# Kernel optimization log

Hardware: AMD Instinct MI355X
Metric: run time of the kernel (lower is better)

The kernel has to match this reference:

```python
import jax, jax.numpy as jnp
import numpy as np

N = 100000
E = 1600000

def _graphconv(x, src, dst, W, b):
    # DGL GraphConv, norm='both', in_feats > out_feats path: transform then aggregate.
    ones = jnp.ones((E,), dtype=x.dtype)
    out_deg = jax.ops.segment_sum(ones, src, num_segments=N)
    in_deg = jax.ops.segment_sum(ones, dst, num_segments=N)
    out_norm = jax.lax.rsqrt(jnp.clip(out_deg, 1.0))  # D_out^{-1/2}
    in_norm = jax.lax.rsqrt(jnp.clip(in_deg, 1.0))    # D_in^{-1/2}
    h = (x * out_norm[:, None]) @ W                    # [N, out_feats]
    msg = h[src]                                       # gather over edges [E, out_feats]
    agg = jax.ops.segment_sum(msg, dst, num_segments=N)
    return agg * in_norm[:, None] + b


def setup_inputs() -> dict:
    key = jax.random.key(0)
    k1, k2, k3, k4, k5 = jax.random.split(key, 5)
    features = jax.random.normal(k1, (N, 256), dtype=jnp.float32)
    src = jax.random.randint(k2, (E,), 0, N, dtype=jnp.int32)
    dst = jax.random.randint(k3, (E,), 0, N, dtype=jnp.int32)
    # Xavier-uniform like DGL's GraphConv reset_parameters
    lim1 = float(np.sqrt(6.0 / (256 + 64)))
    lim2 = float(np.sqrt(6.0 / (64 + 40)))
    W1 = jax.random.uniform(k4, (256, 64), jnp.float32, -lim1, lim1)
    W2 = jax.random.uniform(k5, (64, 40), jnp.float32, -lim2, lim2)
    b1 = jnp.zeros((64,), jnp.float32)
    b2 = jnp.zeros((40,), jnp.float32)
    return {"features": features, "src": src, "dst": dst,
            "W1": W1, "b1": b1, "W2": W2, "b2": b2}


def reference(features, src, dst, W1, b1, W2, b2):
    x = _graphconv(features, src, dst, W1, b1)
    x = _graphconv(x, src, dst, W2, b2)
    return x
```

## Files before the change

### kernel.cpp

```cpp
#include <hip/hip_runtime.h>

#define N_NODES 100000
#define N_EDGES 1600000
#define NBUCK 391
#define HBLK 128


__global__ __launch_bounds__(256) void coarse_hist_kernel(
    const int* __restrict__ src, const int* __restrict__ dst,
    int* __restrict__ gHD, int* __restrict__ gHS) {
    __shared__ int hd[NBUCK], hs[NBUCK];
    for (int i = threadIdx.x; i < NBUCK; i += 256) { hd[i] = 0; hs[i] = 0; }
    __syncthreads();
    for (int e = blockIdx.x * 256 + threadIdx.x; e < N_EDGES; e += HBLK * 256) {
        atomicAdd(&hd[dst[e] >> 8], 1);
        atomicAdd(&hs[src[e] >> 8], 1);
    }
    __syncthreads();
    for (int i = threadIdx.x; i < NBUCK; i += 256) {
        if (hd[i]) atomicAdd(&gHD[i], hd[i]);
        if (hs[i]) atomicAdd(&gHS[i], hs[i]);
    }
}


__global__ void coarse_scan_kernel(const int* __restrict__ gHD, const int* __restrict__ gHS,
                                   int* __restrict__ dBase, int* __restrict__ sBase) {
    __shared__ int sd[512], se[512];
    int t = threadIdx.x;
    int vd = (t < NBUCK) ? gHD[t] : 0;
    int vs = (t < NBUCK) ? gHS[t] : 0;
    sd[t] = vd; se[t] = vs;
    __syncthreads();
    for (int s = 1; s < 512; s <<= 1) {
        int ud = (t >= s) ? sd[t - s] : 0;
        int us = (t >= s) ? se[t - s] : 0;
        __syncthreads();
        sd[t] += ud; se[t] += us;
        __syncthreads();
    }
    if (t < NBUCK) { dBase[t] = sd[t] - vd; sBase[t] = se[t] - vs; }
    if (t == 0) { dBase[NBUCK] = N_EDGES; sBase[NBUCK] = N_EDGES; }
}


__global__ __launch_bounds__(256) void scatter_dst_kernel(
    const int* __restrict__ src, const int* __restrict__ dst,
    const int* __restrict__ dBase, int* __restrict__ dRes,
    int* __restrict__ bsrc, unsigned char* __restrict__ bdlo) {
    __shared__ int h[NBUCK];
    __shared__ int cur[NBUCK];
    for (int i = threadIdx.x; i < NBUCK; i += 256) h[i] = 0;
    __syncthreads();
    for (int e = blockIdx.x * 256 + threadIdx.x; e < N_EDGES; e += HBLK * 256)
        atomicAdd(&h[dst[e] >> 8], 1);
    __syncthreads();
    for (int i = threadIdx.x; i < NBUCK; i += 256) {
        int c = h[i];
        cur[i] = dBase[i] + (c ? atomicAdd(&dRes[i], c) : 0);
    }
    __syncthreads();
    for (int e = blockIdx.x * 256 + threadIdx.x; e < N_EDGES; e += HBLK * 256) {
        int d = dst[e];
        int p = atomicAdd(&cur[d >> 8], 1);
        bsrc[p] = src[e];
        bdlo[p] = (unsigned char)(d & 255);
    }
}


__global__ __launch_bounds__(256) void scatter_src_kernel(
    const int* __restrict__ src,
    const int* __restrict__ sBase, int* __restrict__ sRes,
    unsigned char* __restrict__ bslo) {
    __shared__ int h[NBUCK];
    __shared__ int cur[NBUCK];
    for (int i = threadIdx.x; i < NBUCK; i += 256) h[i] = 0;
    __syncthreads();
    for (int e = blockIdx.x * 256 + threadIdx.x; e < N_EDGES; e += HBLK * 256)
        atomicAdd(&h[src[e] >> 8], 1);
    __syncthreads();
    for (int i = threadIdx.x; i < NBUCK; i += 256) {
        int c = h[i];
        cur[i] = sBase[i] + (c ? atomicAdd(&sRes[i], c) : 0);
    }
    __syncthreads();
    for (int e = blockIdx.x * 256 + threadIdx.x; e < N_EDGES; e += HBLK * 256) {
        int s = src[e];
        int p = atomicAdd(&cur[s >> 8], 1);
        bslo[p] = (unsigned char)(s & 255);
    }
}


__global__ __launch_bounds__(256) void fine_dst_kernel(
    const int* __restrict__ dBase, const unsigned char* __restrict__ bdlo,
    const int* __restrict__ bsrc, int* __restrict__ rs, float* __restrict__ inorm,
    int* __restrict__ ssrc) {
    __shared__ int hist[256], scn[256], cur[256];
    int t = threadIdx.x, b = blockIdx.x;
    int lo = dBase[b], hi = dBase[b + 1];
    hist[t] = 0;
    __syncthreads();
    for (int p = lo + t; p < hi; p += 256) atomicAdd(&hist[bdlo[p]], 1);
    __syncthreads();
    int v = hist[t];
    scn[t] = v;
    __syncthreads();
    for (int s = 1; s < 256; s <<= 1) {
        int u = (t >= s) ? scn[t - s] : 0;
        __syncthreads();
        scn[t] += u;
        __syncthreads();
    }
    int excl = scn[t] - v;
    cur[t] = lo + excl;
    int node = b * 256 + t;
    if (node < N_NODES) {
        rs[node] = lo + excl;
        inorm[node] = 1.0f / sqrtf((float)max(v, 1));
    }
    if (b == 0 && t == 0) rs[N_NODES] = N_EDGES;
    __syncthreads();
    for (int p = lo + t; p < hi; p += 256) {
        int slot = atomicAdd(&cur[bdlo[p]], 1);
        ssrc[slot] = bsrc[p];
    }
}


__global__ __launch_bounds__(256) void fine_src_kernel(
    const int* __restrict__ sBase, const unsigned char* __restrict__ bslo,
    float* __restrict__ onorm) {
    __shared__ int hist[256];
    int t = threadIdx.x, b = blockIdx.x;
    int lo = sBase[b], hi = sBase[b + 1];
    hist[t] = 0;
    __syncthreads();
    for (int p = lo + t; p < hi; p += 256) atomicAdd(&hist[bslo[p]], 1);
    __syncthreads();
    int node = b * 256 + t;
    if (node < N_NODES) onorm[node] = 1.0f / sqrtf((float)max(hist[t], 1));
}


__global__ __launch_bounds__(256) void gemm1_kernel(
    const float* __restrict__ x, const float* __restrict__ W,
    const float* __restrict__ onorm, float* __restrict__ h, int n) {
    __shared__ float As[16][64];
    __shared__ float Ws[16][64];
    const int tid = threadIdx.x;
    const int tx = tid & 15;
    const int ty = tid >> 4;
    const int rowBase = blockIdx.x * 64;

    const int lr = tid >> 2;
    const int lk = (tid & 3) * 4;
    const int lrow = rowBase + lr;
    const bool lvalid = (lrow < n);
    const float lscale = lvalid ? onorm[lrow] : 0.0f;
    const int wk = tid >> 4;
    const int wc = (tid & 15) * 4;

    float acc[4][4] = {};

    for (int k0 = 0; k0 < 256; k0 += 16) {
        float4 v = make_float4(0.f, 0.f, 0.f, 0.f);
        if (lvalid) v = *(const float4*)(x + (size_t)lrow * 256 + k0 + lk);
        As[lk + 0][lr] = v.x * lscale;
        As[lk + 1][lr] = v.y * lscale;
        As[lk + 2][lr] = v.z * lscale;
        As[lk + 3][lr] = v.w * lscale;
        *(float4*)&Ws[wk][wc] = *(const float4*)(W + (size_t)(k0 + wk) * 64 + wc);
        __syncthreads();
#pragma unroll
        for (int k = 0; k < 16; ++k) {
            float4 a = *(const float4*)&As[k][ty * 4];
            float4 b = *(const float4*)&Ws[k][tx * 4];
            float av[4] = {a.x, a.y, a.z, a.w};
            float bv[4] = {b.x, b.y, b.z, b.w};
#pragma unroll
            for (int i = 0; i < 4; ++i)
#pragma unroll
                for (int j = 0; j < 4; ++j) acc[i][j] += av[i] * bv[j];
        }
        __syncthreads();
    }
#pragma unroll
    for (int i = 0; i < 4; ++i) {
        int row = rowBase + ty * 4 + i;
        if (row < n) {
            *(float4*)(h + (size_t)row * 64 + tx * 4) =
                make_float4(acc[i][0], acc[i][1], acc[i][2], acc[i][3]);
        }
    }
}


__global__ __launch_bounds__(256) void agg64_kernel(
    const int* __restrict__ rs, const int* __restrict__ ss,
    const float* __restrict__ h, float* __restrict__ agg, int n) {
    int node = (blockIdx.x * blockDim.x + threadIdx.x) >> 6;
    if (node >= n) return;
    int lane = threadIdx.x & 63;
    int q = lane >> 4;
    int f = lane & 15;
    int beg = rs[node], end = rs[node + 1];
    float4 a0 = {0.f, 0.f, 0.f, 0.f}, a1 = {0.f, 0.f, 0.f, 0.f};
    int j = beg;
    for (; j + 8 <= end; j += 8) {
        int s0 = ss[j + q];
        int s1 = ss[j + 4 + q];
        float4 v0 = *((const float4*)(h + (size_t)s0 * 64) + f);
        float4 v1 = *((const float4*)(h + (size_t)s1 * 64) + f);
        a0.x += v0.x; a0.y += v0.y; a0.z += v0.z; a0.w += v0.w;
        a1.x += v1.x; a1.y += v1.y; a1.z += v1.z; a1.w += v1.w;
    }
    for (; j + 4 <= end; j += 4) {
        int s0 = ss[j + q];
        float4 v0 = *((const float4*)(h + (size_t)s0 * 64) + f);
        a0.x += v0.x; a0.y += v0.y; a0.z += v0.z; a0.w += v0.w;
    }
    if (j + q < end) {
        int s0 = ss[j + q];
        float4 v0 = *((const float4*)(h + (size_t)s0 * 64) + f);
        a0.x += v0.x; a0.y += v0.y; a0.z += v0.z; a0.w += v0.w;
    }
    a0.x += a1.x; a0.y += a1.y; a0.z += a1.z; a0.w += a1.w;
    a0.x += __shfl_xor(a0.x, 16); a0.y += __shfl_xor(a0.y, 16);
    a0.z += __shfl_xor(a0.z, 16); a0.w += __shfl_xor(a0.w, 16);
    a0.x += __shfl_xor(a0.x, 32); a0.y += __shfl_xor(a0.y, 32);
    a0.z += __shfl_xor(a0.z, 32); a0.w += __shfl_xor(a0.w, 32);
    if (q == 0) ((float4*)(agg + (size_t)node * 64))[f] = a0;
}


__global__ __launch_bounds__(256) void gemm2_kernel(
    const float* __restrict__ agg, const float* __restrict__ W2,
    const float* __restrict__ b1, const float* __restrict__ inorm,
    const float* __restrict__ onorm, float* __restrict__ h2, int n) {
    __shared__ float Ws[64 * 40];
    int tid = threadIdx.x;
    for (int i = tid; i < 64 * 40; i += 256) Ws[i] = W2[i];
    __syncthreads();
    int lane = tid & 63;
    int wave = tid >> 6;
    int step = gridDim.x * 4;
    for (int row = blockIdx.x * 4 + wave; row < n; row += step) {
        float so  = onorm[row];
        float s12 = inorm[row] * so;
        const float* ar = agg + (size_t)row * 64;
        if (lane < 40) {
            float acc = 0.f;
#pragma unroll
            for (int k = 0; k < 64; ++k) {
                float xv = ar[k] * s12 + b1[k] * so;
                acc += xv * Ws[k * 40 + lane];
            }
            h2[(size_t)row * 40 + lane] = acc;
        }
    }
}


__global__ __launch_bounds__(256) void agg40_kernel(
    const int* __restrict__ rs, const int* __restrict__ ss,
    const float* __restrict__ h2, const float* __restrict__ inorm,
    const float* __restrict__ b2, float* __restrict__ out, int n) {
    int node = (blockIdx.x * blockDim.x + threadIdx.x) >> 6;
    if (node >= n) return;
    int lane = threadIdx.x & 63;
    int q = lane >> 4;
    int f = lane & 15;
    bool act = (f < 10);
    int beg = rs[node], end = rs[node + 1];
    float4 a0 = {0.f, 0.f, 0.f, 0.f}, a1 = {0.f, 0.f, 0.f, 0.f};
    int j = beg;
    for (; j + 8 <= end; j += 8) {
        int s0 = ss[j + q];
        int s1 = ss[j + 4 + q];
        if (act) {
            float4 v0 = *((const float4*)(h2 + (size_t)s0 * 40) + f);
            float4 v1 = *((const float4*)(h2 + (size_t)s1 * 40) + f);
            a0.x += v0.x; a0.y += v0.y; a0.z += v0.z; a0.w += v0.w;
            a1.x += v1.x; a1.y += v1.y; a1.z += v1.z; a1.w += v1.w;
        }
    }
    for (; j + 4 <= end; j += 4) {
        int s0 = ss[j + q];
        if (act) {
            float4 v0 = *((const float4*)(h2 + (size_t)s0 * 40) + f);
            a0.x += v0.x; a0.y += v0.y; a0.z += v0.z; a0.w += v0.w;
        }
    }
    if (j + q < end && act) {
        int s0 = ss[j + q];
        float4 v0 = *((const float4*)(h2 + (size_t)s0 * 40) + f);
        a0.x += v0.x; a0.y += v0.y; a0.z += v0.z; a0.w += v0.w;
    }
    a0.x += a1.x; a0.y += a1.y; a0.z += a1.z; a0.w += a1.w;
    a0.x += __shfl_xor(a0.x, 16); a0.y += __shfl_xor(a0.y, 16);
    a0.z += __shfl_xor(a0.z, 16); a0.w += __shfl_xor(a0.w, 16);
    a0.x += __shfl_xor(a0.x, 32); a0.y += __shfl_xor(a0.y, 32);
    a0.z += __shfl_xor(a0.z, 32); a0.w += __shfl_xor(a0.w, 32);
    if (q == 0 && act) {
        float s = inorm[node];
        float4 vb = ((const float4*)b2)[f];
        float4 r;
        r.x = a0.x * s + vb.x; r.y = a0.y * s + vb.y;
        r.z = a0.z * s + vb.z; r.w = a0.w * s + vb.w;
        ((float4*)(out + (size_t)node * 40))[f] = r;
    }
}

extern "C" void kernel_launch(void* const* d_in, const int* in_sizes, int n_in,
                              void* d_out, int out_size, void* d_ws, size_t ws_size,
                              hipStream_t stream) {
    const float* x  = (const float*)d_in[0];
    const int* src  = (const int*)d_in[1];
    const int* dst  = (const int*)d_in[2];
    const float* W1 = (const float*)d_in[3];
    const float* b1 = (const float*)d_in[4];
    const float* W2 = (const float*)d_in[5];
    const float* b2 = (const float*)d_in[6];
    float* out = (float*)d_out;

    char* wsb = (char*)d_ws;
    size_t off = 0;
    auto alloc = [&](size_t bytes) { char* p = wsb + off; off += (bytes + 255) & ~size_t(255); return p; };

    int*   zeroed = (int*)  alloc(4 * NBUCK * 4);
    int*   gHD    = zeroed;
    int*   gHS    = zeroed + NBUCK;
    int*   dRes   = zeroed + 2 * NBUCK;
    int*   sRes   = zeroed + 3 * NBUCK;
    int*   dBase  = (int*)  alloc((NBUCK + 1) * 4);
    int*   sBase  = (int*)  alloc((NBUCK + 1) * 4);
    float* onorm  = (float*)alloc(N_NODES * 4);
    float* inorm  = (float*)alloc(N_NODES * 4);
    int*   rs     = (int*)  alloc((N_NODES + 1) * 4);
    int*   ssrc   = (int*)  alloc((size_t)N_EDGES * 4);
    float* h1     = (float*)alloc((size_t)N_NODES * 64 * 4);
    float* agg1   = (float*)alloc((size_t)N_NODES * 64 * 4);
    float* h2 = h1;
    int* bsrc = (int*)agg1;
    unsigned char* bdlo = (unsigned char*)(bsrc + N_EDGES);
    unsigned char* bslo = bdlo + N_EDGES;

    hipMemsetAsync(zeroed, 0, 4 * NBUCK * 4, stream);

    coarse_hist_kernel<<<HBLK, 256, 0, stream>>>(src, dst, gHD, gHS);
    coarse_scan_kernel<<<1, 512, 0, stream>>>(gHD, gHS, dBase, sBase);
    scatter_dst_kernel<<<HBLK, 256, 0, stream>>>(src, dst, dBase, dRes, bsrc, bdlo);
    scatter_src_kernel<<<HBLK, 256, 0, stream>>>(src, sBase, sRes, bslo);
    fine_dst_kernel<<<NBUCK, 256, 0, stream>>>(dBase, bdlo, bsrc, rs, inorm, ssrc);
    fine_src_kernel<<<NBUCK, 256, 0, stream>>>(sBase, bslo, onorm);

    gemm1_kernel<<<(N_NODES + 63) / 64, 256, 0, stream>>>(x, W1, onorm, h1, N_NODES);

    agg64_kernel<<<(N_NODES * 64) / 256, 256, 0, stream>>>(rs, ssrc, h1, agg1, N_NODES);

    gemm2_kernel<<<2048, 256, 0, stream>>>(agg1, W2, b1, inorm, onorm, h2, N_NODES);

    agg40_kernel<<<(N_NODES * 64) / 256, 256, 0, stream>>>(rs, ssrc, h2, inorm, b2, out, N_NODES);
}
```

Measured before the change: 484.8 us.

## Rewrite both dense GEMMs as wave-per-row-tile kernels with register-resident weights

The first GEMM drops its LDS-tiled 64x64 scheme. Each wave now computes 16 rows, one output column per lane, reading x rows as wave-uniform broadcast loads and W columns straight from global memory. The out-norm scale moves to the epilogue. The second GEMM keeps the whole W2 column in 64 registers per lane and folds the bias term into a per-column constant c2, then uses a one-shot grid of 8 rows per wave in place of a grid-stride loop. The goal is to remove LDS traffic and synchronisation, but the change raises register pressure and relies on scalar or broadcast global loads for x and agg.

```diff
diff --git a/kernel.cpp b/kernel.cpp
--- a/kernel.cpp
+++ b/kernel.cpp
@@ -147,51 +147,35 @@
 __global__ __launch_bounds__(256) void gemm1_kernel(
     const float* __restrict__ x, const float* __restrict__ W,
     const float* __restrict__ onorm, float* __restrict__ h, int n) {
-    __shared__ float As[16][64];
-    __shared__ float Ws[16][64];
-    const int tid = threadIdx.x;
-    const int tx = tid & 15;
-    const int ty = tid >> 4;
-    const int rowBase = blockIdx.x * 64;
-
-    const int lr = tid >> 2;
-    const int lk = (tid & 3) * 4;
-    const int lrow = rowBase + lr;
-    const bool lvalid = (lrow < n);
-    const float lscale = lvalid ? onorm[lrow] : 0.0f;
-    const int wk = tid >> 4;
-    const int wc = (tid & 15) * 4;
-
-    float acc[4][4] = {};
-
-    for (int k0 = 0; k0 < 256; k0 += 16) {
-        float4 v = make_float4(0.f, 0.f, 0.f, 0.f);
-        if (lvalid) v = *(const float4*)(x + (size_t)lrow * 256 + k0 + lk);
-        As[lk + 0][lr] = v.x * lscale;
-        As[lk + 1][lr] = v.y * lscale;
-        As[lk + 2][lr] = v.z * lscale;
-        As[lk + 3][lr] = v.w * lscale;
-        *(float4*)&Ws[wk][wc] = *(const float4*)(W + (size_t)(k0 + wk) * 64 + wc);
-        __syncthreads();
-#pragma unroll
-        for (int k = 0; k < 16; ++k) {
-            float4 a = *(const float4*)&As[k][ty * 4];
-            float4 b = *(const float4*)&Ws[k][tx * 4];
-            float av[4] = {a.x, a.y, a.z, a.w};
-            float bv[4] = {b.x, b.y, b.z, b.w};
-#pragma unroll
-            for (int i = 0; i < 4; ++i)
-#pragma unroll
-                for (int j = 0; j < 4; ++j) acc[i][j] += av[i] * bv[j];
-        }
-        __syncthreads();
-    }
-#pragma unroll
-    for (int i = 0; i < 4; ++i) {
-        int row = rowBase + ty * 4 + i;
+    const int lane = threadIdx.x & 63;
+    const int wid = __builtin_amdgcn_readfirstlane(threadIdx.x >> 6);
+    const int rowBase = (blockIdx.x * 4 + wid) * 16;
+
+    float acc[16];
+#pragma unroll
+    for (int r = 0; r < 16; ++r) acc[r] = 0.f;
+
+    for (int kc = 0; kc < 256; kc += 4) {
+        float w0 = W[(size_t)(kc + 0) * 64 + lane];
+        float w1 = W[(size_t)(kc + 1) * 64 + lane];
+        float w2 = W[(size_t)(kc + 2) * 64 + lane];
+        float w3 = W[(size_t)(kc + 3) * 64 + lane];
+#pragma unroll
+        for (int r = 0; r < 16; ++r) {
+            int row = rowBase + r;
+            if (row < n) {
+                const float* xr = x + (size_t)row * 256 + kc;
+                float a0 = xr[0], a1 = xr[1], a2 = xr[2], a3 = xr[3];
+                acc[r] += a0 * w0 + a1 * w1 + a2 * w2 + a3 * w3;
+            }
+        }
+    }
+#pragma unroll
+    for (int r = 0; r < 16; ++r) {
+        int row = rowBase + r;
         if (row < n) {
-            *(float4*)(h + (size_t)row * 64 + tx * 4) =
-                make_float4(acc[i][0], acc[i][1], acc[i][2], acc[i][3]);
+            float s = onorm[row];
+            h[(size_t)row * 64 + lane] = acc[r] * s;
         }
     }
 }
@@ -239,25 +223,30 @@
     const float* __restrict__ agg, const float* __restrict__ W2,
     const float* __restrict__ b1, const float* __restrict__ inorm,
     const float* __restrict__ onorm, float* __restrict__ h2, int n) {
-    __shared__ float Ws[64 * 40];
-    int tid = threadIdx.x;
-    for (int i = tid; i < 64 * 40; i += 256) Ws[i] = W2[i];
-    __syncthreads();
-    int lane = tid & 63;
-    int wave = tid >> 6;
-    int step = gridDim.x * 4;
-    for (int row = blockIdx.x * 4 + wave; row < n; row += step) {
-        float so  = onorm[row];
-        float s12 = inorm[row] * so;
-        const float* ar = agg + (size_t)row * 64;
-        if (lane < 40) {
+    const int lane = threadIdx.x & 63;
+    const int wid = __builtin_amdgcn_readfirstlane(threadIdx.x >> 6);
+    const int rowBase = (blockIdx.x * 4 + wid) * 8;
+    const int cl = lane < 40 ? lane : 39;
+
+    float w[64];
+#pragma unroll
+    for (int k = 0; k < 64; ++k) w[k] = W2[k * 40 + cl];
+
+    float c2 = 0.f;
+#pragma unroll
+    for (int k = 0; k < 64; ++k) c2 += b1[k] * w[k];
+
+#pragma unroll
+    for (int r = 0; r < 8; ++r) {
+        int row = rowBase + r;
+        if (row < n) {
+            const float* ar = agg + (size_t)row * 64;
             float acc = 0.f;
 #pragma unroll
-            for (int k = 0; k < 64; ++k) {
-                float xv = ar[k] * s12 + b1[k] * so;
-                acc += xv * Ws[k * 40 + lane];
-            }
-            h2[(size_t)row * 40 + lane] = acc;
+            for (int k = 0; k < 64; ++k) acc += ar[k] * w[k];
+            float so = onorm[row];
+            float s12 = inorm[row] * so;
+            if (lane < 40) h2[(size_t)row * 40 + lane] = acc * s12 + so * c2;
         }
     }
 }
@@ -360,7 +349,7 @@
 
     agg64_kernel<<<(N_NODES * 64) / 256, 256, 0, stream>>>(rs, ssrc, h1, agg1, N_NODES);
 
-    gemm2_kernel<<<2048, 256, 0, stream>>>(agg1, W2, b1, inorm, onorm, h2, N_NODES);
+    gemm2_kernel<<<(N_NODES + 31) / 32, 256, 0, stream>>>(agg1, W2, b1, inorm, onorm, h2, N_NODES);
 
     agg40_kernel<<<(N_NODES * 64) / 256, 256, 0, stream>>>(rs, ssrc, h2, inorm, b2, out, N_NODES);
 }
```

New measurement: 942.8 us. 94.4% more time.
